# Optimization experiments

Measured on AMD Instinct MI355X. Metric: run time of the kernel, lower is better.

## Reference

```python
import jax, jax.numpy as jnp
import numpy as np

N = 100000   # nodes
E = 3200000  # edges
F = 128      # input features
H = 6        # hiddenSize
C = 10       # num_classes
G = 512      # graphs in batch


def setup_inputs() -> dict:
    key = jax.random.key(0)
    ks = jax.random.split(key, 13)
    x = jax.random.normal(ks[0], (N, F), dtype=jnp.float32)
    edge_index = jax.random.randint(ks[1], (2, E), 0, N, dtype=jnp.int32)
    batch = jnp.sort(jax.random.randint(ks[2], (N,), 0, G, dtype=jnp.int32))

    def lin(k, fan_in, fan_out):
        return jax.random.normal(k, (fan_in, fan_out), dtype=jnp.float32) / np.sqrt(fan_in).astype(np.float32)

    return {
        "x": x, "edge_index": edge_index, "batch": batch,
        "W1": lin(ks[3], F, H), "b1": jnp.zeros((H,), jnp.float32),
        "W2": lin(ks[4], H, H), "b2": jnp.zeros((H,), jnp.float32),
        "W3": lin(ks[5], H, H), "b3": jnp.zeros((H,), jnp.float32),
        "W4": lin(ks[6], H, H), "b4": jnp.zeros((H,), jnp.float32),
        "Wf": lin(ks[7], H, C), "bf": jnp.zeros((C,), jnp.float32),
    }


def _gcn_conv(x, W, b, src, dst, norm):
    # x' = scatter_add_{dst}( norm * (x W)[src] ) + b   (GCNConv, sym-norm, self-loops)
    h = x @ W
    msg = norm[:, None] * h[src]
    return jax.ops.segment_sum(msg, dst, num_segments=N) + b


def reference(x, edge_index, batch, W1, b1, W2, b2, W3, b3, W4, b4, Wf, bf):
    loops = jnp.arange(N, dtype=edge_index.dtype)
    src = jnp.concatenate([edge_index[0], loops])
    dst = jnp.concatenate([edge_index[1], loops])
    # degree (with self-loops) at the aggregation side, symmetric normalization
    deg = jax.ops.segment_sum(jnp.ones_like(dst, dtype=jnp.float32), dst, num_segments=N)
    dinv = jnp.where(deg > 0, jax.lax.rsqrt(deg), 0.0)
    norm = dinv[src] * dinv[dst]

    h = jax.nn.relu(_gcn_conv(x, W1, b1, src, dst, norm))
    h = jax.nn.relu(_gcn_conv(h, W2, b2, src, dst, norm))
    h = jax.nn.relu(_gcn_conv(h, W3, b3, src, dst, norm))
    h = jax.nn.relu(_gcn_conv(h, W4, b4, src, dst, norm))
    h = jax.nn.relu(_gcn_conv(h, Wf, bf, src, dst, norm))  # [N, C]

    # global_mean_pool over graph ids
    sums = jax.ops.segment_sum(h, batch, num_segments=G)          # [G, C]
    counts = jax.ops.segment_sum(jnp.ones((N,), jnp.float32), batch, num_segments=G)
    pooled = sums / jnp.maximum(counts, 1.0)[:, None]
    return jax.nn.log_softmax(pooled, axis=1)
```

## Files before the change

### kernel.cpp

```cpp
#include <hip/hip_runtime.h>
#include <math.h>

#define NN 100000
#define EE 3200000
#define FF 128
#define HH 6
#define CC 10
#define GG 512
#define NBUCK 196
#define BCAP 20000
#define PTILE 4096

typedef _Float16 half8 __attribute__((ext_vector_type(8)));

__global__ __launch_bounds__(256) void k_initcur(int* __restrict__ gcur) {
    int t = threadIdx.x;
    if (t < NBUCK) gcur[t] = t * BCAP;
}

__global__ __launch_bounds__(256) void k_partition(const int* __restrict__ src,
                                                   const int* __restrict__ dst,
                                                   int* __restrict__ gcur,
                                                   int* __restrict__ part) {
    __shared__ int lcnt[NBUCK], lbase[NBUCK], lpos[NBUCK];
    int t = threadIdx.x;
    for (int i = t; i < NBUCK; i += 256) { lcnt[i] = 0; lpos[i] = 0; }
    __syncthreads();
    int base = blockIdx.x * PTILE;
    int d[16];
#pragma unroll
    for (int k = 0; k < 16; ++k) {
        int e = base + (k << 8) + t;
        d[k] = (e < EE) ? dst[e] : -1;
    }
#pragma unroll
    for (int k = 0; k < 16; ++k)
        if (d[k] >= 0) atomicAdd(&lcnt[d[k] >> 9], 1);
    __syncthreads();
    for (int i = t; i < NBUCK; i += 256)
        lbase[i] = lcnt[i] ? atomicAdd(&gcur[i], lcnt[i]) : 0;
    __syncthreads();
    int s[16];
#pragma unroll
    for (int k = 0; k < 16; ++k) {
        int e = base + (k << 8) + t;
        s[k] = (e < EE) ? src[e] : 0;
    }
#pragma unroll
    for (int k = 0; k < 16; ++k) {
        if (d[k] >= 0) {
            int bkt = d[k] >> 9;
            int r = atomicAdd(&lpos[bkt], 1);
            part[lbase[bkt] + r] = (s[k] << 9) | (d[k] & 511);
        }
    }
}

__global__ __launch_bounds__(512) void k_bucketfill(const int* __restrict__ gcur,
                                                    const int* __restrict__ part,
                                                    int* __restrict__ csr,
                                                    int* __restrict__ rowptr,
                                                    int* __restrict__ counts,
                                                    float* __restrict__ dinv) {
    __shared__ int cnt[512], scn[512], cur[512];
    int t = threadIdx.x;
    int b = blockIdx.x;
    int nbase = b << 9;
    int ebase = b * BCAP, ecount = gcur[b] - ebase;
    cnt[t] = 0;
    __syncthreads();
    for (int j = t; j < ecount; j += 512)
        atomicAdd(&cnt[part[ebase + j] & 511], 1);
    __syncthreads();
    int c = cnt[t];
    scn[t] = c;
    __syncthreads();
    for (int off = 1; off < 512; off <<= 1) {
        int u = (t >= off) ? scn[t - off] : 0;
        __syncthreads();
        scn[t] += u;
        __syncthreads();
    }
    int rp = ebase + scn[t] - c;
    int node = nbase + t;
    if (node < NN) {
        rowptr[node] = rp;
        counts[node] = c;
        dinv[node] = rsqrtf((float)c + 1.0f);
    }
    cur[t] = rp;
    __syncthreads();
    for (int j = t; j < ecount; j += 512) {
        int p = part[ebase + j];
        int pos = atomicAdd(&cur[p & 511], 1);
        csr[pos] = p >> 9;
    }
}

__global__ __launch_bounds__(256) void k_xw1(const float* __restrict__ x,
                                             const float* __restrict__ W,
                                             const float* __restrict__ dinv,
                                             _Float16* __restrict__ hs) {
    __shared__ float sW[FF * HH];
    for (int i = threadIdx.x; i < FF * HH; i += 256) sW[i] = W[i];
    __syncthreads();
    int node = blockIdx.x * 64 + (threadIdx.x >> 2);
    int sub  = threadIdx.x & 3;
    if (node >= NN) return;
    const float4* xr = (const float4*)(x + (size_t)node * FF + sub * 32);
    float acc[HH];
#pragma unroll
    for (int c = 0; c < HH; ++c) acc[c] = 0.f;
#pragma unroll
    for (int q = 0; q < 8; ++q) {
        float4 v = xr[q];
        int k = sub * 32 + q * 4;
        const float* w0 = &sW[(k + 0) * HH];
        const float* w1 = &sW[(k + 1) * HH];
        const float* w2 = &sW[(k + 2) * HH];
        const float* w3 = &sW[(k + 3) * HH];
#pragma unroll
        for (int c = 0; c < HH; ++c)
            acc[c] += v.x * w0[c] + v.y * w1[c] + v.z * w2[c] + v.w * w3[c];
    }
#pragma unroll
    for (int c = 0; c < HH; ++c) {
        acc[c] += __shfl_xor(acc[c], 1, 64);
        acc[c] += __shfl_xor(acc[c], 2, 64);
    }
    if (sub == 0) {
        float di = dinv[node];
        half8 o;
#pragma unroll
        for (int c = 0; c < HH; ++c) o[c] = (_Float16)(di * acc[c]);
        o[6] = (_Float16)0.f; o[7] = (_Float16)0.f;
        *((half8*)(hs + (size_t)node * 8)) = o;
    }
}

template <int HON, int HPOH>
__global__ __launch_bounds__(256) void k_gf(const int* __restrict__ rowptr,
                                            const int* __restrict__ counts,
                                            const int* __restrict__ csr,
                                            const float* __restrict__ dinv,
                                            const _Float16* __restrict__ hs,
                                            const float* __restrict__ bias,
                                            const float* __restrict__ Wn,
                                            _Float16* __restrict__ outn) {
    __shared__ float sW[HH * HON];
    if (threadIdx.x < HH * HON) sW[threadIdx.x] = Wn[threadIdx.x];
    __syncthreads();
    int node = blockIdx.x * 64 + (threadIdx.x >> 2);
    int sub  = threadIdx.x & 3;
    if (node >= NN) return;
    int st = rowptr[node], cnt = counts[node];
    float a[HH];
    if (sub == 0) {
        half8 v = *((const half8*)(hs + (size_t)node * 8));
#pragma unroll
        for (int c = 0; c < HH; ++c) a[c] = (float)v[c];
    } else {
#pragma unroll
        for (int c = 0; c < HH; ++c) a[c] = 0.f;
    }
    int j = st + sub, end = st + cnt;
    for (; j + 4 < end; j += 8) {
        int s0 = csr[j], s1 = csr[j + 4];
        half8 v0 = *((const half8*)(hs + (size_t)s0 * 8));
        half8 v1 = *((const half8*)(hs + (size_t)s1 * 8));
#pragma unroll
        for (int c = 0; c < HH; ++c) a[c] += (float)v0[c] + (float)v1[c];
    }
    if (j < end) {
        int s = csr[j];
        half8 v = *((const half8*)(hs + (size_t)s * 8));
#pragma unroll
        for (int c = 0; c < HH; ++c) a[c] += (float)v[c];
    }
#pragma unroll
    for (int c = 0; c < HH; ++c) {
        a[c] += __shfl_xor(a[c], 1, 64);
        a[c] += __shfl_xor(a[c], 2, 64);
    }
    if (sub == 0) {
        float di = dinv[node];
        float h[HH];
#pragma unroll
        for (int c = 0; c < HH; ++c) h[c] = fmaxf(di * a[c] + bias[c], 0.f);
        half8 o[HPOH / 8];
#pragma unroll
        for (int c = 0; c < HPOH; ++c) {
            float s = 0.f;
            if (c < HON) {
#pragma unroll
                for (int k = 0; k < HH; ++k) s += h[k] * sW[k * HON + c];
                o[c / 8][c % 8] = (_Float16)(di * s);
            } else {
                o[c / 8][c % 8] = (_Float16)0.f;
            }
        }
        half8* op = (half8*)(outn + (size_t)node * HPOH);
#pragma unroll
        for (int q = 0; q < HPOH / 8; ++q) op[q] = o[q];
    }
}

__global__ __launch_bounds__(256) void k_glast(const int* __restrict__ rowptr,
                                               const int* __restrict__ counts,
                                               const int* __restrict__ csr,
                                               const float* __restrict__ dinv,
                                               const _Float16* __restrict__ hs,
                                               const float* __restrict__ bias,
                                               float* __restrict__ out) {
    int node = blockIdx.x * 64 + (threadIdx.x >> 2);
    int sub  = threadIdx.x & 3;
    if (node >= NN) return;
    int st = rowptr[node], cnt = counts[node];
    float a[CC];
    if (sub == 0) {
        const half8* p = (const half8*)(hs + (size_t)node * 16);
        half8 v0 = p[0], v1 = p[1];
#pragma unroll
        for (int c = 0; c < 8; ++c) a[c] = (float)v0[c];
        a[8] = (float)v1[0]; a[9] = (float)v1[1];
    } else {
#pragma unroll
        for (int c = 0; c < CC; ++c) a[c] = 0.f;
    }
    int j = st + sub, end = st + cnt;
    for (; j + 4 < end; j += 8) {
        int s0 = csr[j], s1 = csr[j + 4];
        const half8* p0 = (const half8*)(hs + (size_t)s0 * 16);
        const half8* p1 = (const half8*)(hs + (size_t)s1 * 16);
        half8 x0 = p0[0], y0 = p0[1], x1 = p1[0], y1 = p1[1];
#pragma unroll
        for (int c = 0; c < 8; ++c) a[c] += (float)x0[c] + (float)x1[c];
        a[8] += (float)y0[0] + (float)y1[0];
        a[9] += (float)y0[1] + (float)y1[1];
    }
    if (j < end) {
        int s = csr[j];
        const half8* p = (const half8*)(hs + (size_t)s * 16);
        half8 x0 = p[0], y0 = p[1];
#pragma unroll
        for (int c = 0; c < 8; ++c) a[c] += (float)x0[c];
        a[8] += (float)y0[0]; a[9] += (float)y0[1];
    }
#pragma unroll
    for (int c = 0; c < CC; ++c) {
        a[c] += __shfl_xor(a[c], 1, 64);
        a[c] += __shfl_xor(a[c], 2, 64);
    }
    if (sub == 0) {
        float di = dinv[node];
        float r[12];
#pragma unroll
        for (int c = 0; c < 12; ++c)
            r[c] = (c < CC) ? fmaxf(di * a[c] + bias[c], 0.f) : 0.f;
        float4* o = (float4*)(out + (size_t)node * 12);
        o[0] = make_float4(r[0], r[1], r[2], r[3]);
        o[1] = make_float4(r[4], r[5], r[6], r[7]);
        o[2] = make_float4(r[8], r[9], r[10], r[11]);
    }
}

__global__ __launch_bounds__(256) void k_bounds(const int* __restrict__ batch,
                                                int* __restrict__ bounds) {
    int g = blockIdx.x * 256 + threadIdx.x;
    if (g > GG) return;
    int lo = 0, hi = NN;
    while (lo < hi) {
        int mid = (lo + hi) >> 1;
        if (batch[mid] < g) lo = mid + 1; else hi = mid;
    }
    bounds[g] = lo;
}

__global__ __launch_bounds__(256) void k_pool(const float* __restrict__ h,
                                              const int* __restrict__ bounds,
                                              float* __restrict__ out) {
    int g = blockIdx.x;
    int s = bounds[g], e = bounds[g + 1];
    float acc[CC];
#pragma unroll
    for (int c = 0; c < CC; ++c) acc[c] = 0.f;
    for (int i = s + threadIdx.x; i < e; i += 256) {
#pragma unroll
        for (int c = 0; c < CC; ++c) acc[c] += h[(size_t)i * 12 + c];
    }
#pragma unroll
    for (int off = 32; off >= 1; off >>= 1)
#pragma unroll
        for (int c = 0; c < CC; ++c) acc[c] += __shfl_down(acc[c], off, 64);
    __shared__ float sacc[4][CC];
    int wv = threadIdx.x >> 6, lane = threadIdx.x & 63;
    if (lane == 0) {
#pragma unroll
        for (int c = 0; c < CC; ++c) sacc[wv][c] = acc[c];
    }
    __syncthreads();
    if (threadIdx.x == 0) {
        float cnt = fmaxf((float)(e - s), 1.0f);
        float tot[CC];
        float m = -1e30f;
#pragma unroll
        for (int c = 0; c < CC; ++c) {
            tot[c] = (sacc[0][c] + sacc[1][c] + sacc[2][c] + sacc[3][c]) / cnt;
            m = fmaxf(m, tot[c]);
        }
        float ssum = 0.f;
#pragma unroll
        for (int c = 0; c < CC; ++c) ssum += expf(tot[c] - m);
        float lse = logf(ssum) + m;
#pragma unroll
        for (int c = 0; c < CC; ++c) out[(size_t)g * CC + c] = tot[c] - lse;
    }
}

extern "C" void kernel_launch(void* const* d_in, const int* in_sizes, int n_in,
                              void* d_out, int out_size, void* d_ws, size_t ws_size,
                              hipStream_t stream) {
    const float* x     = (const float*)d_in[0];
    const int*   ei    = (const int*)d_in[1];
    const int*   batch = (const int*)d_in[2];
    const float* W1 = (const float*)d_in[3];
    const float* b1 = (const float*)d_in[4];
    const float* W2 = (const float*)d_in[5];
    const float* b2 = (const float*)d_in[6];
    const float* W3 = (const float*)d_in[7];
    const float* b3 = (const float*)d_in[8];
    const float* W4 = (const float*)d_in[9];
    const float* b4 = (const float*)d_in[10];
    const float* Wf = (const float*)d_in[11];
    const float* bf = (const float*)d_in[12];
    float* out = (float*)d_out;

    const int* src = ei;
    const int* dst = ei + EE;

    int*   iw     = (int*)d_ws;
    int*   csr    = iw;
    int*   rowptr = csr + 3920000;
    int*   counts = rowptr + 100352;
    float* dinv   = (float*)(counts + 100352);
    int*   gcur   = (int*)(dinv + 100352);
    int*   bounds = gcur + 256;
    int*   part   = bounds + 640;
    _Float16* hsA = (_Float16*)part;
    _Float16* hsB = hsA + 1605632;
    float* h5     = (float*)(hsB + 1605632);

    const int TB = (EE + PTILE - 1) / PTILE;
    const int GB = (NN + 63) / 64;

    k_initcur<<<1, 256, 0, stream>>>(gcur);
    k_partition<<<TB, 256, 0, stream>>>(src, dst, gcur, part);
    k_bucketfill<<<NBUCK, 512, 0, stream>>>(gcur, part, csr, rowptr, counts, dinv);

    k_xw1<<<GB, 256, 0, stream>>>(x, W1, dinv, hsA);
    k_gf<HH, 8><<<GB, 256, 0, stream>>>(rowptr, counts, csr, dinv, hsA, b1, W2, hsB);
    k_gf<HH, 8><<<GB, 256, 0, stream>>>(rowptr, counts, csr, dinv, hsB, b2, W3, hsA);
    k_gf<HH, 8><<<GB, 256, 0, stream>>>(rowptr, counts, csr, dinv, hsA, b3, W4, hsB);
    k_gf<CC, 16><<<GB, 256, 0, stream>>>(rowptr, counts, csr, dinv, hsB, b4, Wf, hsA);
    k_glast<<<GB, 256, 0, stream>>>(rowptr, counts, csr, dinv, hsA, bf, h5);

    k_bounds<<<3, 256, 0, stream>>>(batch, bounds);
    k_pool<<<GG, 256, 0, stream>>>(h5, bounds, out);
}
```

Baseline: 223.5 us.

## Single-pass atomic ranking in CSR build and fuse mean-pool into last layer

The partition kernel keeps the rank returned by the counting atomic and reuses it for placement, dropping the second atomic pass. The bucket fill uses 1024 threads, holds its edges in registers, and replaces the shared-memory scan with a wavefront shuffle scan. The last GCN layer now atomically accumulates relu outputs into per-graph sums instead of writing an intermediate node array, and a tiny kernel finishes the mean and log-softmax. Atomic contention on per-graph sums (sorted batch) and register pressure from the MAXIT arrays are the risks.

```diff
diff --git a/kernel.cpp b/kernel.cpp
--- a/kernel.cpp
+++ b/kernel.cpp
@@ -9,7 +9,8 @@
 #define GG 512
 #define NBUCK 196
 #define BCAP 20000
-#define PTILE 4096
+#define PTILE 2048
+#define MAXIT 20
 
 typedef _Float16 half8 __attribute__((ext_vector_type(8)));
 
@@ -22,79 +23,83 @@
                                                    const int* __restrict__ dst,
                                                    int* __restrict__ gcur,
                                                    int* __restrict__ part) {
-    __shared__ int lcnt[NBUCK], lbase[NBUCK], lpos[NBUCK];
+    __shared__ int lcnt[NBUCK], lbase[NBUCK];
     int t = threadIdx.x;
-    for (int i = t; i < NBUCK; i += 256) { lcnt[i] = 0; lpos[i] = 0; }
+    for (int i = t; i < NBUCK; i += 256) lcnt[i] = 0;
     __syncthreads();
     int base = blockIdx.x * PTILE;
-    int d[16];
-#pragma unroll
-    for (int k = 0; k < 16; ++k) {
+    int d[8], s[8], r[8];
+#pragma unroll
+    for (int k = 0; k < 8; ++k) {
         int e = base + (k << 8) + t;
         d[k] = (e < EE) ? dst[e] : -1;
-    }
-#pragma unroll
-    for (int k = 0; k < 16; ++k)
-        if (d[k] >= 0) atomicAdd(&lcnt[d[k] >> 9], 1);
+        s[k] = (e < EE) ? src[e] : 0;
+    }
+#pragma unroll
+    for (int k = 0; k < 8; ++k)
+        if (d[k] >= 0) r[k] = atomicAdd(&lcnt[d[k] >> 9], 1);
     __syncthreads();
     for (int i = t; i < NBUCK; i += 256)
         lbase[i] = lcnt[i] ? atomicAdd(&gcur[i], lcnt[i]) : 0;
     __syncthreads();
-    int s[16];
-#pragma unroll
-    for (int k = 0; k < 16; ++k) {
-        int e = base + (k << 8) + t;
-        s[k] = (e < EE) ? src[e] : 0;
-    }
-#pragma unroll
-    for (int k = 0; k < 16; ++k) {
+#pragma unroll
+    for (int k = 0; k < 8; ++k) {
         if (d[k] >= 0) {
             int bkt = d[k] >> 9;
-            int r = atomicAdd(&lpos[bkt], 1);
-            part[lbase[bkt] + r] = (s[k] << 9) | (d[k] & 511);
+            part[lbase[bkt] + r[k]] = (s[k] << 9) | (d[k] & 511);
         }
     }
 }
 
-__global__ __launch_bounds__(512) void k_bucketfill(const int* __restrict__ gcur,
-                                                    const int* __restrict__ part,
-                                                    int* __restrict__ csr,
-                                                    int* __restrict__ rowptr,
-                                                    int* __restrict__ counts,
-                                                    float* __restrict__ dinv) {
-    __shared__ int cnt[512], scn[512], cur[512];
-    int t = threadIdx.x;
-    int b = blockIdx.x;
+__global__ __launch_bounds__(1024) void k_bucketfill(const int* __restrict__ gcur,
+                                                     const int* __restrict__ part,
+                                                     int* __restrict__ csr,
+                                                     int* __restrict__ rowptr,
+                                                     int* __restrict__ counts,
+                                                     float* __restrict__ dinv) {
+    __shared__ int cnt[512];
+    __shared__ int wsum[16];
+    int t = threadIdx.x, b = blockIdx.x;
     int nbase = b << 9;
     int ebase = b * BCAP, ecount = gcur[b] - ebase;
-    cnt[t] = 0;
-    __syncthreads();
-    for (int j = t; j < ecount; j += 512)
-        atomicAdd(&cnt[part[ebase + j] & 511], 1);
-    __syncthreads();
-    int c = cnt[t];
-    scn[t] = c;
-    __syncthreads();
-    for (int off = 1; off < 512; off <<= 1) {
-        int u = (t >= off) ? scn[t - off] : 0;
-        __syncthreads();
-        scn[t] += u;
-        __syncthreads();
-    }
-    int rp = ebase + scn[t] - c;
-    int node = nbase + t;
-    if (node < NN) {
-        rowptr[node] = rp;
-        counts[node] = c;
-        dinv[node] = rsqrtf((float)c + 1.0f);
-    }
-    cur[t] = rp;
-    __syncthreads();
-    for (int j = t; j < ecount; j += 512) {
-        int p = part[ebase + j];
-        int pos = atomicAdd(&cur[p & 511], 1);
-        csr[pos] = p >> 9;
-    }
+    if (t < 512) cnt[t] = 0;
+    __syncthreads();
+    int p[MAXIT], r[MAXIT];
+#pragma unroll
+    for (int it = 0; it < MAXIT; ++it) {
+        int j = (it << 10) + t;
+        p[it] = (j < ecount) ? part[ebase + j] : -1;
+    }
+#pragma unroll
+    for (int it = 0; it < MAXIT; ++it)
+        if (p[it] >= 0) r[it] = atomicAdd(&cnt[p[it] & 511], 1);
+    __syncthreads();
+    int c = (t < 512) ? cnt[t] : 0;
+    int lane = t & 63, wv = t >> 6;
+    int v = c;
+#pragma unroll
+    for (int off = 1; off < 64; off <<= 1) {
+        int u = __shfl_up(v, off, 64);
+        if (lane >= off) v += u;
+    }
+    if (lane == 63) wsum[wv] = v;
+    __syncthreads();
+    int acc = 0;
+    for (int k = 0; k < wv; ++k) acc += wsum[k];
+    int excl = ebase + acc + v - c;
+    if (t < 512) {
+        int node = nbase + t;
+        if (node < NN) {
+            rowptr[node] = excl;
+            counts[node] = c;
+            dinv[node] = rsqrtf((float)c + 1.0f);
+        }
+        cnt[t] = excl;
+    }
+    __syncthreads();
+#pragma unroll
+    for (int it = 0; it < MAXIT; ++it)
+        if (p[it] >= 0) csr[cnt[p[it] & 511] + r[it]] = p[it] >> 9;
 }
 
 __global__ __launch_bounds__(256) void k_xw1(const float* __restrict__ x,
@@ -211,7 +216,8 @@
                                                const float* __restrict__ dinv,
                                                const _Float16* __restrict__ hs,
                                                const float* __restrict__ bias,
-                                               float* __restrict__ out) {
+                                               const int* __restrict__ batch,
+                                               float* __restrict__ gpool) {
     int node = blockIdx.x * 64 + (threadIdx.x >> 2);
     int sub  = threadIdx.x & 3;
     if (node >= NN) return;
@@ -253,14 +259,13 @@
     }
     if (sub == 0) {
         float di = dinv[node];
-        float r[12];
-#pragma unroll
-        for (int c = 0; c < 12; ++c)
-            r[c] = (c < CC) ? fmaxf(di * a[c] + bias[c], 0.f) : 0.f;
-        float4* o = (float4*)(out + (size_t)node * 12);
-        o[0] = make_float4(r[0], r[1], r[2], r[3]);
-        o[1] = make_float4(r[4], r[5], r[6], r[7]);
-        o[2] = make_float4(r[8], r[9], r[10], r[11]);
+        int g = batch[node];
+        float* gp = gpool + (size_t)g * CC;
+#pragma unroll
+        for (int c = 0; c < CC; ++c) {
+            float rv = fmaxf(di * a[c] + bias[c], 0.f);
+            atomicAdd(&gp[c], rv);
+        }
     }
 }
 
@@ -276,45 +281,25 @@
     bounds[g] = lo;
 }
 
-__global__ __launch_bounds__(256) void k_pool(const float* __restrict__ h,
-                                              const int* __restrict__ bounds,
-                                              float* __restrict__ out) {
-    int g = blockIdx.x;
-    int s = bounds[g], e = bounds[g + 1];
-    float acc[CC];
-#pragma unroll
-    for (int c = 0; c < CC; ++c) acc[c] = 0.f;
-    for (int i = s + threadIdx.x; i < e; i += 256) {
-#pragma unroll
-        for (int c = 0; c < CC; ++c) acc[c] += h[(size_t)i * 12 + c];
-    }
-#pragma unroll
-    for (int off = 32; off >= 1; off >>= 1)
-#pragma unroll
-        for (int c = 0; c < CC; ++c) acc[c] += __shfl_down(acc[c], off, 64);
-    __shared__ float sacc[4][CC];
-    int wv = threadIdx.x >> 6, lane = threadIdx.x & 63;
-    if (lane == 0) {
-#pragma unroll
-        for (int c = 0; c < CC; ++c) sacc[wv][c] = acc[c];
-    }
-    __syncthreads();
-    if (threadIdx.x == 0) {
-        float cnt = fmaxf((float)(e - s), 1.0f);
-        float tot[CC];
-        float m = -1e30f;
-#pragma unroll
-        for (int c = 0; c < CC; ++c) {
-            tot[c] = (sacc[0][c] + sacc[1][c] + sacc[2][c] + sacc[3][c]) / cnt;
-            m = fmaxf(m, tot[c]);
-        }
-        float ssum = 0.f;
-#pragma unroll
-        for (int c = 0; c < CC; ++c) ssum += expf(tot[c] - m);
-        float lse = logf(ssum) + m;
-#pragma unroll
-        for (int c = 0; c < CC; ++c) out[(size_t)g * CC + c] = tot[c] - lse;
-    }
+__global__ __launch_bounds__(256) void k_poolfin(const float* __restrict__ gpool,
+                                                 const int* __restrict__ bounds,
+                                                 float* __restrict__ out) {
+    int g = blockIdx.x * 256 + threadIdx.x;
+    if (g >= GG) return;
+    float cntf = fmaxf((float)(bounds[g + 1] - bounds[g]), 1.0f);
+    float tot[CC];
+    float m = -1e30f;
+#pragma unroll
+    for (int c = 0; c < CC; ++c) {
+        tot[c] = gpool[(size_t)g * CC + c] / cntf;
+        m = fmaxf(m, tot[c]);
+    }
+    float ss = 0.f;
+#pragma unroll
+    for (int c = 0; c < CC; ++c) ss += expf(tot[c] - m);
+    float lse = logf(ss) + m;
+#pragma unroll
+    for (int c = 0; c < CC; ++c) out[(size_t)g * CC + c] = tot[c] - lse;
 }
 
 extern "C" void kernel_launch(void* const* d_in, const int* in_sizes, int n_in,
@@ -345,25 +330,26 @@
     float* dinv   = (float*)(counts + 100352);
     int*   gcur   = (int*)(dinv + 100352);
     int*   bounds = gcur + 256;
-    int*   part   = bounds + 640;
+    float* gpool  = (float*)(bounds + 640);
+    int*   part   = (int*)(gpool + 5376);
     _Float16* hsA = (_Float16*)part;
     _Float16* hsB = hsA + 1605632;
-    float* h5     = (float*)(hsB + 1605632);
 
     const int TB = (EE + PTILE - 1) / PTILE;
     const int GB = (NN + 63) / 64;
 
     k_initcur<<<1, 256, 0, stream>>>(gcur);
+    hipMemsetAsync(gpool, 0, GG * CC * sizeof(float), stream);
+    k_bounds<<<3, 256, 0, stream>>>(batch, bounds);
     k_partition<<<TB, 256, 0, stream>>>(src, dst, gcur, part);
-    k_bucketfill<<<NBUCK, 512, 0, stream>>>(gcur, part, csr, rowptr, counts, dinv);
+    k_bucketfill<<<NBUCK, 1024, 0, stream>>>(gcur, part, csr, rowptr, counts, dinv);
 
     k_xw1<<<GB, 256, 0, stream>>>(x, W1, dinv, hsA);
     k_gf<HH, 8><<<GB, 256, 0, stream>>>(rowptr, counts, csr, dinv, hsA, b1, W2, hsB);
     k_gf<HH, 8><<<GB, 256, 0, stream>>>(rowptr, counts, csr, dinv, hsB, b2, W3, hsA);
     k_gf<HH, 8><<<GB, 256, 0, stream>>>(rowptr, counts, csr, dinv, hsA, b3, W4, hsB);
     k_gf<CC, 16><<<GB, 256, 0, stream>>>(rowptr, counts, csr, dinv, hsB, b4, Wf, hsA);
-    k_glast<<<GB, 256, 0, stream>>>(rowptr, counts, csr, dinv, hsA, bf, h5);
-
-    k_bounds<<<3, 256, 0, stream>>>(batch, bounds);
-    k_pool<<<GG, 256, 0, stream>>>(h5, bounds, out);
-}
+    k_glast<<<GB, 256, 0, stream>>>(rowptr, counts, csr, dinv, hsA, bf, batch, gpool);
+
+    k_poolfin<<<2, 256, 0, stream>>>(gpool, bounds, out);
+}
```

After: 471.7 us. +111.1%, slower.
